# Optimization experiments

Hardware: AMD Instinct MI355X
Metric: run time of the kernel (lower is better)

Reference implementation:

```python
import jax, jax.numpy as jnp
import numpy as np

CHAMFER_WEIGHT = 1.0
PC_NUM_WEIGHT = 0.1


def setup_inputs() -> dict:
    key = jax.random.key(0)
    k1, k2, k3, k4, k5 = jax.random.split(key, 5)
    B, D, H, W = 4, 20, 128, 128
    pred_coor = jax.random.normal(k1, (B, 3 * D, H, W), dtype=jnp.float32)
    gt_coor = jax.random.normal(k2, (B, D, 3, H, W), dtype=jnp.float32)
    chamfer_mask = (jax.random.uniform(k3, (B, D, H, W)) < 0.7).astype(jnp.float32)
    gt_mask = jnp.ones((B, H, W), dtype=jnp.float32)
    pred_num = jax.random.normal(k4, (B, 1, H, W), dtype=jnp.float32)
    gt_num = jax.random.normal(k5, (B, 1, H, W), dtype=jnp.float32)
    return {"pred_coor": pred_coor, "gt_coor": gt_coor, "chamfer_mask": chamfer_mask,
            "gt_mask": gt_mask, "pred_num": pred_num, "gt_num": gt_num}


def _chamfer(pred_coor, gt_coor, chamfer_mask, gt_mask):
    B, _, H, W = pred_coor.shape
    D = gt_coor.shape[1]
    # src: [B,3*D,H,W] -> [K,3,D] -> [K,D,3]  (matches torch reshape(-1,3,20).permute(0,2,1))
    src = pred_coor.transpose(0, 2, 3, 1).reshape(-1, 3, D).transpose(0, 2, 1)
    # dst: [B,D,3,H,W] -> [B,D*3,H,W] -> [K,D,3]
    dst = gt_coor.reshape(B, D * 3, H, W).transpose(0, 2, 3, 1).reshape(-1, D, 3)
    cm = chamfer_mask.transpose(0, 2, 3, 1).reshape(-1, D)  # [K,D]
    vw = gt_mask.reshape(-1)  # [K] voxel selection weight (binary)

    # L1 pairwise distance, summed over coordinate axis: [K,D,D]
    dist = jnp.abs(src[:, :, None, :] - dst[:, None, :, :]).sum(-1)
    max_d = jax.lax.stop_gradient(
        jnp.max(jnp.where(vw[:, None, None] > 0, dist, -jnp.inf)))
    s2d = jnp.min(dist - cm[:, None, :] * max_d, axis=2) + max_d  # [K,D]
    d2s = jnp.min(dist, axis=1)                                    # [K,D]

    wsum = vw.sum()
    loss_src = (s2d * vw[:, None]).sum() / (wsum * D)             # mean over selected
    denom = (cm * vw[:, None]).sum()
    loss_dst = (d2s * cm * vw[:, None]).sum() / denom
    return loss_src + loss_dst


def _num_loss(pred_num, gt_num, gt_mask):
    diff = pred_num - gt_num
    ad = jnp.abs(diff)
    sl1 = jnp.where(ad < 1.0, 0.5 * diff * diff, ad - 0.5)  # smooth_l1, beta=1
    sl1 = sl1.squeeze(1)  # [B,H,W]
    return (sl1 * gt_mask).sum() / gt_mask.sum()


def reference(pred_coor, gt_coor, chamfer_mask, gt_mask, pred_num, gt_num):
    chamfer_loss = _chamfer(pred_coor, gt_coor, chamfer_mask, gt_mask)
    pc_num_loss = _num_loss(pred_num, gt_num, gt_mask)
    return CHAMFER_WEIGHT * chamfer_loss + PC_NUM_WEIGHT * pc_num_loss
```

## Files before the change

### kernel.cpp

```cpp
#include <hip/hip_runtime.h>
#include <stdint.h>

#define HW     16384
#define NTILES 1024
#define INFI   0x7f800000

__global__ __launch_bounds__(512, 6) void chamfer_main(
    const float* __restrict__ pred,
    const float* __restrict__ gt,
    const float* __restrict__ cmask,
    const float* __restrict__ vmask,
    const float* __restrict__ pnum,
    const float* __restrict__ gnum,
    float* __restrict__ ws)
{
    __shared__ int rm_m[20][64];
    __shared__ int rm_a[20][64];
    __shared__ int cd_s[20][64];
    __shared__ int mx_s[64];
    __shared__ int bt_s[64];

    const int tid  = threadIdx.x;
    const int lane = tid & 63;
    const int w    = tid >> 6;
    const int ri   = w >> 2;
    const int cj   = w & 3;
    const int i0   = ri * 10, j0 = cj * 5;
    const int k    = blockIdx.x * 64 + lane;
    const int b    = k >> 14;
    const int hw   = k & (HW - 1);
    const size_t pb = (size_t)b * 60 * HW + hw;
    const size_t cb = (size_t)b * 20 * HW + hw;

    float dxv[5], dyv[5], dzv[5], cmf[5];
    #pragma unroll
    for (int jj = 0; jj < 5; ++jj) {
        dxv[jj] = gt[pb + (size_t)(3 * (j0 + jj)    ) * HW];
        dyv[jj] = gt[pb + (size_t)(3 * (j0 + jj) + 1) * HW];
        dzv[jj] = gt[pb + (size_t)(3 * (j0 + jj) + 2) * HW];
        cmf[jj] = cmask[cb + (size_t)(j0 + jj) * HW];
    }
    float vw = 0.f, pn = 0.f, gn = 0.f;
    if (w == 0) { vw = vmask[k]; pn = pnum[k]; gn = gnum[k]; }

    {
        int* pm = &rm_m[0][0]; int* pa = &rm_a[0][0]; int* pc = &cd_s[0][0];
        for (int t = tid; t < 1280; t += 512) { pm[t] = INFI; pa[t] = INFI; pc[t] = INFI; }
        if (tid < 64) { mx_s[tid] = 0; bt_s[tid] = 0; }
    }
    __syncthreads();

    unsigned mybits = 0u;
    #pragma unroll
    for (int jj = 0; jj < 5; ++jj)
        if (cmf[jj] > 0.f) mybits |= 1u << jj;
    if (ri == 0 && mybits) atomicOr(&bt_s[lane], (int)(mybits << j0));

    const float INF = __int_as_float(INFI);
    float rmm[10], rma[10], cds[5], mx = 0.f;
    #pragma unroll
    for (int t = 0; t < 10; ++t) { rmm[t] = INF; rma[t] = INF; }
    #pragma unroll
    for (int t = 0; t < 5; ++t) cds[t] = INF;

    #pragma unroll
    for (int r = 0; r < 10; ++r) {
        const int i = i0 + r;
        const float sx = pred[pb + (size_t)(i)      * HW];
        const float sy = pred[pb + (size_t)(20 + i) * HW];
        const float sz = pred[pb + (size_t)(40 + i) * HW];
        #pragma unroll
        for (int jj = 0; jj < 5; ++jj) {
            float d = fabsf(sx - dxv[jj]) + fabsf(sy - dyv[jj]) + fabsf(sz - dzv[jj]);
            mx      = fmaxf(mx, d);
            cds[jj] = fminf(cds[jj], d);
            rma[r]  = fminf(rma[r], d);
            rmm[r]  = fminf(rmm[r], (cmf[jj] > 0.f) ? d : INF);
        }
    }

    #pragma unroll
    for (int r = 0; r < 10; ++r) {
        atomicMin(&rm_m[i0 + r][lane], __float_as_int(rmm[r]));
        atomicMin(&rm_a[i0 + r][lane], __float_as_int(rma[r]));
    }
    #pragma unroll
    for (int jj = 0; jj < 5; ++jj)
        atomicMin(&cd_s[j0 + jj][lane], __float_as_int(cds[jj]));
    atomicMax(&mx_s[lane], __float_as_int(mx));
    __syncthreads();

    if (w == 0) {
        const unsigned cmbits = (unsigned)bt_s[lane];
        float srcA = 0.f;
        #pragma unroll
        for (int i = 0; i < 20; ++i) {
            const int vm_ = rm_m[i][lane];
            const int va_ = rm_a[i][lane];
            srcA += __int_as_float(cmbits ? vm_ : va_);
        }
        float dsum = 0.f;
        #pragma unroll
        for (int j = 0; j < 20; ++j)
            if ((cmbits >> j) & 1u) dsum += __int_as_float(cd_s[j][lane]);
        const float mxv = __int_as_float(mx_s[lane]);

        float vals[7];
        vals[0] = srcA * vw;
        vals[1] = (cmbits == 0u) ? 20.f * vw : 0.f;
        vals[2] = dsum * vw;
        vals[3] = vw * (float)__popc(cmbits);
        const float diff = pn - gn;
        const float ad = fabsf(diff);
        vals[4] = ((ad < 1.f) ? 0.5f * diff * diff : (ad - 0.5f)) * vw;
        vals[5] = vw;
        vals[6] = (vw > 0.f) ? mxv : 0.f;

        #pragma unroll
        for (int o = 32; o > 0; o >>= 1) {
            #pragma unroll
            for (int x = 0; x < 6; ++x) vals[x] += __shfl_down(vals[x], o);
            vals[6] = fmaxf(vals[6], __shfl_down(vals[6], o));
        }
        if (lane == 0) {
            float* rec = ws + (size_t)blockIdx.x * 8;
            #pragma unroll
            for (int x = 0; x < 7; ++x) rec[x] = vals[x];
        }
    }
}

__global__ __launch_bounds__(256) void chamfer_fin(
    const float* __restrict__ ws, float* __restrict__ out)
{
    __shared__ float red[4][8];
    const int tid  = threadIdx.x;
    const int lane = tid & 63;
    const int wv   = tid >> 6;
    float a[6] = {0.f, 0.f, 0.f, 0.f, 0.f, 0.f};
    float mx = 0.f;
    for (int r = tid; r < NTILES; r += 256) {
        const float* rec = ws + (size_t)r * 8;
        #pragma unroll
        for (int v = 0; v < 6; ++v) a[v] += rec[v];
        mx = fmaxf(mx, rec[6]);
    }
    #pragma unroll
    for (int o = 32; o > 0; o >>= 1) {
        #pragma unroll
        for (int v = 0; v < 6; ++v) a[v] += __shfl_down(a[v], o);
        mx = fmaxf(mx, __shfl_down(mx, o));
    }
    if (lane == 0) {
        #pragma unroll
        for (int v = 0; v < 6; ++v) red[wv][v] = a[v];
        red[wv][6] = mx;
    }
    __syncthreads();
    if (tid == 0) {
        #pragma unroll
        for (int v = 0; v < 6; ++v) a[v] = red[0][v] + red[1][v] + red[2][v] + red[3][v];
        mx = fmaxf(fmaxf(red[0][6], red[1][6]), fmaxf(red[2][6], red[3][6]));
        const float loss_s = (a[0] + a[1] * mx) / (a[5] * 20.f);
        const float loss_d = a[2] / a[3];
        const float numl   = a[4] / a[5];
        out[0] = loss_s + loss_d + 0.1f * numl;
    }
}

extern "C" void kernel_launch(void* const* d_in, const int* in_sizes, int n_in,
                              void* d_out, int out_size, void* d_ws, size_t ws_size,
                              hipStream_t stream)
{
    const float* pred  = (const float*)d_in[0];
    const float* gt    = (const float*)d_in[1];
    const float* cmask = (const float*)d_in[2];
    const float* vmask = (const float*)d_in[3];
    const float* pnum  = (const float*)d_in[4];
    const float* gnum  = (const float*)d_in[5];
    float* out = (float*)d_out;
    float* ws  = (float*)d_ws;

    chamfer_main<<<NTILES, 512, 0, stream>>>(pred, gt, cmask, vmask, pnum, gnum, ws);
    chamfer_fin<<<1, 256, 0, stream>>>(ws, out);
}
```

Baseline: 18.28 us.

## Fuse final reduction via last-block atomic counter and drop all-distance row mins

Removes the separate finalize kernel: each block writes its partial record, bumps an atomic counter, and the last block reduces all records and writes the output. A memset of the counter is added before launch. It also drops the second unmasked row-min array and recomputes it lazily only for voxels whose chamfer mask row is all-zero, and raises the launch-bounds occupancy hint. The counter is stored at ws+7, which is slot 7 of block 0's record; that slot is never written by the record store, so it does not conflict. A leftover unused chamfer_main kernel remains in the file.

After: 51.15 us. 2.8x slower.

```diff
diff --git a/kernel.cpp b/kernel.cpp
--- a/kernel.cpp
+++ b/kernel.cpp
@@ -5,7 +5,7 @@
 #define NTILES 1024
 #define INFI   0x7f800000
 
-__global__ __launch_bounds__(512, 6) void chamfer_main(
+__global__ __launch_bounds__(512, 8) void chamfer_main(
     const float* __restrict__ pred,
     const float* __restrict__ gt,
     const float* __restrict__ cmask,
@@ -15,7 +15,6 @@
     float* __restrict__ ws)
 {
     __shared__ int rm_m[20][64];
-    __shared__ int rm_a[20][64];
     __shared__ int cd_s[20][64];
     __shared__ int mx_s[64];
     __shared__ int bt_s[64];
@@ -44,8 +43,8 @@
     if (w == 0) { vw = vmask[k]; pn = pnum[k]; gn = gnum[k]; }
 
     {
-        int* pm = &rm_m[0][0]; int* pa = &rm_a[0][0]; int* pc = &cd_s[0][0];
-        for (int t = tid; t < 1280; t += 512) { pm[t] = INFI; pa[t] = INFI; pc[t] = INFI; }
+        int* pm = &rm_m[0][0]; int* pc = &cd_s[0][0];
+        for (int t = tid; t < 1280; t += 512) { pm[t] = INFI; pc[t] = INFI; }
         if (tid < 64) { mx_s[tid] = 0; bt_s[tid] = 0; }
     }
     __syncthreads();
@@ -57,9 +56,9 @@
     if (ri == 0 && mybits) atomicOr(&bt_s[lane], (int)(mybits << j0));
 
     const float INF = __int_as_float(INFI);
-    float rmm[10], rma[10], cds[5], mx = 0.f;
-    #pragma unroll
-    for (int t = 0; t < 10; ++t) { rmm[t] = INF; rma[t] = INF; }
+    float rmm[10], cds[5], mx = 0.f;
+    #pragma unroll
+    for (int t = 0; t < 10; ++t) rmm[t] = INF;
     #pragma unroll
     for (int t = 0; t < 5; ++t) cds[t] = INF;
 
@@ -74,31 +73,43 @@
             float d = fabsf(sx - dxv[jj]) + fabsf(sy - dyv[jj]) + fabsf(sz - dzv[jj]);
             mx      = fmaxf(mx, d);
             cds[jj] = fminf(cds[jj], d);
-            rma[r]  = fminf(rma[r], d);
             rmm[r]  = fminf(rmm[r], (cmf[jj] > 0.f) ? d : INF);
         }
     }
 
     #pragma unroll
-    for (int r = 0; r < 10; ++r) {
+    for (int r = 0; r < 10; ++r)
         atomicMin(&rm_m[i0 + r][lane], __float_as_int(rmm[r]));
-        atomicMin(&rm_a[i0 + r][lane], __float_as_int(rma[r]));
-    }
     #pragma unroll
     for (int jj = 0; jj < 5; ++jj)
         atomicMin(&cd_s[j0 + jj][lane], __float_as_int(cds[jj]));
     atomicMax(&mx_s[lane], __float_as_int(mx));
     __syncthreads();
 
+    if (__any(bt_s[lane] == 0)) {
+        if (bt_s[lane] == 0) {
+            #pragma unroll
+            for (int r = 0; r < 10; ++r) {
+                const int i = i0 + r;
+                const float sx = pred[pb + (size_t)(i)      * HW];
+                const float sy = pred[pb + (size_t)(20 + i) * HW];
+                const float sz = pred[pb + (size_t)(40 + i) * HW];
+                float rm = INF;
+                #pragma unroll
+                for (int jj = 0; jj < 5; ++jj)
+                    rm = fminf(rm, fabsf(sx - dxv[jj]) + fabsf(sy - dyv[jj])
+                                 + fabsf(sz - dzv[jj]));
+                atomicMin(&rm_m[i][lane], __float_as_int(rm));
+            }
+        }
+        __syncthreads();
+    }
+
     if (w == 0) {
         const unsigned cmbits = (unsigned)bt_s[lane];
         float srcA = 0.f;
         #pragma unroll
-        for (int i = 0; i < 20; ++i) {
-            const int vm_ = rm_m[i][lane];
-            const int va_ = rm_a[i][lane];
-            srcA += __int_as_float(cmbits ? vm_ : va_);
-        }
+        for (int i = 0; i < 20; ++i) srcA += __int_as_float(rm_m[i][lane]);
         float dsum = 0.f;
         #pragma unroll
         for (int j = 0; j < 20; ++j)
@@ -127,44 +138,201 @@
             #pragma unroll
             for (int x = 0; x < 7; ++x) rec[x] = vals[x];
         }
+
+        unsigned old = 0;
+        if (lane == 0) {
+            __threadfence();
+            old = atomicAdd((unsigned*)(ws + 7), 1u);
+        }
+        old = __shfl(old, 0);
+        if (old == NTILES - 1) {
+            __threadfence();
+            float a[6] = {0.f, 0.f, 0.f, 0.f, 0.f, 0.f};
+            float fmx = 0.f;
+            for (int r = lane; r < NTILES; r += 64) {
+                const float* rec = ws + (size_t)r * 8;
+                #pragma unroll
+                for (int v = 0; v < 6; ++v) a[v] += rec[v];
+                fmx = fmaxf(fmx, rec[6]);
+            }
+            #pragma unroll
+            for (int o = 32; o > 0; o >>= 1) {
+                #pragma unroll
+                for (int v = 0; v < 6; ++v) a[v] += __shfl_down(a[v], o);
+                fmx = fmaxf(fmx, __shfl_down(fmx, o));
+            }
+            if (lane == 0) {
+                const float loss_s = (a[0] + a[1] * fmx) / (a[5] * 20.f);
+                const float loss_d = a[2] / a[3];
+                const float numl   = a[4] / a[5];
+                float* outp = (float*)((char*)ws - 0);
+                (void)outp;
+            }
+        }
     }
 }
 
-__global__ __launch_bounds__(256) void chamfer_fin(
-    const float* __restrict__ ws, float* __restrict__ out)
+
+__global__ __launch_bounds__(512, 8) void chamfer_all(
+    const float* __restrict__ pred, const float* __restrict__ gt,
+    const float* __restrict__ cmask, const float* __restrict__ vmask,
+    const float* __restrict__ pnum, const float* __restrict__ gnum,
+    float* __restrict__ ws, float* __restrict__ out)
 {
-    __shared__ float red[4][8];
+    __shared__ int rm_m[20][64];
+    __shared__ int cd_s[20][64];
+    __shared__ int mx_s[64];
+    __shared__ int bt_s[64];
+
     const int tid  = threadIdx.x;
     const int lane = tid & 63;
-    const int wv   = tid >> 6;
-    float a[6] = {0.f, 0.f, 0.f, 0.f, 0.f, 0.f};
-    float mx = 0.f;
-    for (int r = tid; r < NTILES; r += 256) {
-        const float* rec = ws + (size_t)r * 8;
-        #pragma unroll
-        for (int v = 0; v < 6; ++v) a[v] += rec[v];
-        mx = fmaxf(mx, rec[6]);
-    }
-    #pragma unroll
-    for (int o = 32; o > 0; o >>= 1) {
-        #pragma unroll
-        for (int v = 0; v < 6; ++v) a[v] += __shfl_down(a[v], o);
-        mx = fmaxf(mx, __shfl_down(mx, o));
-    }
-    if (lane == 0) {
-        #pragma unroll
-        for (int v = 0; v < 6; ++v) red[wv][v] = a[v];
-        red[wv][6] = mx;
+    const int w    = tid >> 6;
+    const int ri   = w >> 2;
+    const int cj   = w & 3;
+    const int i0   = ri * 10, j0 = cj * 5;
+    const int k    = blockIdx.x * 64 + lane;
+    const int b    = k >> 14;
+    const int hw   = k & (HW - 1);
+    const size_t pb = (size_t)b * 60 * HW + hw;
+    const size_t cb = (size_t)b * 20 * HW + hw;
+
+    float dxv[5], dyv[5], dzv[5], cmf[5];
+    #pragma unroll
+    for (int jj = 0; jj < 5; ++jj) {
+        dxv[jj] = gt[pb + (size_t)(3 * (j0 + jj)    ) * HW];
+        dyv[jj] = gt[pb + (size_t)(3 * (j0 + jj) + 1) * HW];
+        dzv[jj] = gt[pb + (size_t)(3 * (j0 + jj) + 2) * HW];
+        cmf[jj] = cmask[cb + (size_t)(j0 + jj) * HW];
+    }
+    float vw = 0.f, pn = 0.f, gn = 0.f;
+    if (w == 0) { vw = vmask[k]; pn = pnum[k]; gn = gnum[k]; }
+
+    {
+        int* pm = &rm_m[0][0]; int* pc = &cd_s[0][0];
+        for (int t = tid; t < 1280; t += 512) { pm[t] = INFI; pc[t] = INFI; }
+        if (tid < 64) { mx_s[tid] = 0; bt_s[tid] = 0; }
     }
     __syncthreads();
-    if (tid == 0) {
-        #pragma unroll
-        for (int v = 0; v < 6; ++v) a[v] = red[0][v] + red[1][v] + red[2][v] + red[3][v];
-        mx = fmaxf(fmaxf(red[0][6], red[1][6]), fmaxf(red[2][6], red[3][6]));
-        const float loss_s = (a[0] + a[1] * mx) / (a[5] * 20.f);
-        const float loss_d = a[2] / a[3];
-        const float numl   = a[4] / a[5];
-        out[0] = loss_s + loss_d + 0.1f * numl;
+
+    unsigned mybits = 0u;
+    #pragma unroll
+    for (int jj = 0; jj < 5; ++jj)
+        if (cmf[jj] > 0.f) mybits |= 1u << jj;
+    if (ri == 0 && mybits) atomicOr(&bt_s[lane], (int)(mybits << j0));
+
+    const float INF = __int_as_float(INFI);
+    float rmm[10], cds[5], mx = 0.f;
+    #pragma unroll
+    for (int t = 0; t < 10; ++t) rmm[t] = INF;
+    #pragma unroll
+    for (int t = 0; t < 5; ++t) cds[t] = INF;
+
+    #pragma unroll
+    for (int r = 0; r < 10; ++r) {
+        const int i = i0 + r;
+        const float sx = pred[pb + (size_t)(i)      * HW];
+        const float sy = pred[pb + (size_t)(20 + i) * HW];
+        const float sz = pred[pb + (size_t)(40 + i) * HW];
+        #pragma unroll
+        for (int jj = 0; jj < 5; ++jj) {
+            float d = fabsf(sx - dxv[jj]) + fabsf(sy - dyv[jj]) + fabsf(sz - dzv[jj]);
+            mx      = fmaxf(mx, d);
+            cds[jj] = fminf(cds[jj], d);
+            rmm[r]  = fminf(rmm[r], (cmf[jj] > 0.f) ? d : INF);
+        }
+    }
+
+    #pragma unroll
+    for (int r = 0; r < 10; ++r)
+        atomicMin(&rm_m[i0 + r][lane], __float_as_int(rmm[r]));
+    #pragma unroll
+    for (int jj = 0; jj < 5; ++jj)
+        atomicMin(&cd_s[j0 + jj][lane], __float_as_int(cds[jj]));
+    atomicMax(&mx_s[lane], __float_as_int(mx));
+    __syncthreads();
+
+    if (__any(bt_s[lane] == 0)) {
+        if (bt_s[lane] == 0) {
+            #pragma unroll
+            for (int r = 0; r < 10; ++r) {
+                const int i = i0 + r;
+                const float sx = pred[pb + (size_t)(i)      * HW];
+                const float sy = pred[pb + (size_t)(20 + i) * HW];
+                const float sz = pred[pb + (size_t)(40 + i) * HW];
+                float rm = INF;
+                #pragma unroll
+                for (int jj = 0; jj < 5; ++jj)
+                    rm = fminf(rm, fabsf(sx - dxv[jj]) + fabsf(sy - dyv[jj])
+                                 + fabsf(sz - dzv[jj]));
+                atomicMin(&rm_m[i][lane], __float_as_int(rm));
+            }
+        }
+        __syncthreads();
+    }
+
+    if (w == 0) {
+        const unsigned cmbits = (unsigned)bt_s[lane];
+        float srcA = 0.f;
+        #pragma unroll
+        for (int i = 0; i < 20; ++i) srcA += __int_as_float(rm_m[i][lane]);
+        float dsum = 0.f;
+        #pragma unroll
+        for (int j = 0; j < 20; ++j)
+            if ((cmbits >> j) & 1u) dsum += __int_as_float(cd_s[j][lane]);
+        const float mxv = __int_as_float(mx_s[lane]);
+
+        float vals[7];
+        vals[0] = srcA * vw;
+        vals[1] = (cmbits == 0u) ? 20.f * vw : 0.f;
+        vals[2] = dsum * vw;
+        vals[3] = vw * (float)__popc(cmbits);
+        const float diff = pn - gn;
+        const float ad = fabsf(diff);
+        vals[4] = ((ad < 1.f) ? 0.5f * diff * diff : (ad - 0.5f)) * vw;
+        vals[5] = vw;
+        vals[6] = (vw > 0.f) ? mxv : 0.f;
+
+        #pragma unroll
+        for (int o = 32; o > 0; o >>= 1) {
+            #pragma unroll
+            for (int x = 0; x < 6; ++x) vals[x] += __shfl_down(vals[x], o);
+            vals[6] = fmaxf(vals[6], __shfl_down(vals[6], o));
+        }
+        if (lane == 0) {
+            float* rec = ws + (size_t)blockIdx.x * 8;
+            #pragma unroll
+            for (int x = 0; x < 7; ++x) rec[x] = vals[x];
+        }
+
+        unsigned old = 0;
+        if (lane == 0) {
+            __threadfence();
+            old = atomicAdd((unsigned*)(ws + 7), 1u);
+        }
+        old = __shfl(old, 0);
+        if (old == NTILES - 1) {
+            __threadfence();
+            float a[6] = {0.f, 0.f, 0.f, 0.f, 0.f, 0.f};
+            float fmx = 0.f;
+            for (int r = lane; r < NTILES; r += 64) {
+                const float* rec = ws + (size_t)r * 8;
+                #pragma unroll
+                for (int v = 0; v < 6; ++v) a[v] += rec[v];
+                fmx = fmaxf(fmx, rec[6]);
+            }
+            #pragma unroll
+            for (int o = 32; o > 0; o >>= 1) {
+                #pragma unroll
+                for (int v = 0; v < 6; ++v) a[v] += __shfl_down(a[v], o);
+                fmx = fmaxf(fmx, __shfl_down(fmx, o));
+            }
+            if (lane == 0) {
+                const float loss_s = (a[0] + a[1] * fmx) / (a[5] * 20.f);
+                const float loss_d = a[2] / a[3];
+                const float numl   = a[4] / a[5];
+                out[0] = loss_s + loss_d + 0.1f * numl;
+            }
+        }
     }
 }
 
@@ -181,6 +349,6 @@
     float* out = (float*)d_out;
     float* ws  = (float*)d_ws;
 
-    chamfer_main<<<NTILES, 512, 0, stream>>>(pred, gt, cmask, vmask, pnum, gnum, ws);
-    chamfer_fin<<<1, 256, 0, stream>>>(ws, out);
+    hipMemsetAsync(ws + 7, 0, 4, stream);
+    chamfer_all<<<NTILES, 512, 0, stream>>>(pred, gt, cmask, vmask, pnum, gnum, ws, out);
 }
```
